# Optimization experiments

Hardware: AMD Instinct MI355X
Metric: run time of the kernel (lower is better)

Reference implementation:

```python
import jax, jax.numpy as jnp
import numpy as np

# config (stands in for global `args` in the original repo)
N = 8192            # args.tRNA + args.disease
NNZ = 262144        # number of edges in adj
N_SEEDS = 256
MASK_DEPTH = 2      # args.maskDepth
KEEP_RATE = 0.9     # args.keepRate


def setup_inputs() -> dict:
    rng = np.random.default_rng(0)
    # duplicate-free edge list (coalesced sparse tensor)
    h = rng.choice(N * N, size=NNZ, replace=False)
    adj_rows = jnp.asarray(h // N, dtype=jnp.int32)
    adj_cols = jnp.asarray(h % N, dtype=jnp.int32)
    key = jax.random.key(0)
    k1, k2, k3 = jax.random.split(key, 3)
    adj_values = jax.random.uniform(k1, (NNZ,), dtype=jnp.float32)
    seeds = jax.random.randint(k2, (N_SEEDS,), 0, N, dtype=jnp.int32)
    complemental = jax.random.uniform(k3, (N, N), dtype=jnp.float32)
    return {"adj_rows": adj_rows, "adj_cols": adj_cols, "adj_values": adj_values,
            "seeds": seeds, "complemental": complemental}


def _forward(adj_rows, adj_cols, adj_values, seeds, complemental):
    rows, cols = adj_rows, adj_cols
    # --- BFS edge masking (sequential per-seed removal == union removal) ---
    keep = jnp.ones((NNZ,), bool)
    seed_mask = jnp.zeros((N,), bool).at[seeds].set(True)
    mask_nodes = seed_mask
    for i in range(MASK_DEPTH):
        incident = keep & (seed_mask[rows] | seed_mask[cols])
        keep = keep & ~incident
        if i != MASK_DEPTH - 1:
            inc_i = incident.astype(jnp.int32)
            nxt = (jnp.zeros((N,), jnp.int32).at[rows].add(inc_i)
                   .at[cols].add(inc_i)) > 0
            seed_mask = nxt
            mask_nodes = mask_nodes | nxt
    # --- random node sampling augments the mask set ---
    key = jax.random.key(42)
    k1, k2, k3 = jax.random.split(key, 3)
    samp_num = int(N * KEEP_RATE)
    samped = jax.random.randint(k1, (samp_num,), 0, N)
    mask_nodes = mask_nodes.at[samped].set(True)
    # --- encoder adj: kept edges, values gathered from complemental, D^-1/2 A D^-1/2 ---
    keep_i = keep.astype(jnp.int32)
    enc_cov = (jnp.zeros((N, N), jnp.int32).at[rows, cols].add(keep_i)) > 0
    enc_dense = jnp.where(enc_cov, complemental, 0.0)
    deg = enc_dense.sum(axis=1)
    norm = (deg + 1e-12) ** -0.5
    enc = enc_dense * norm[:, None] * norm[None, :]
    # --- decoder adj: random mask-node pairs (symmetric) + self loops + kept edges ---
    mask_idx = jnp.nonzero(mask_nodes, size=N, fill_value=0)[0]
    tem_num = mask_nodes.sum()
    u1 = jax.random.uniform(k2, (NNZ,))
    u2 = jax.random.uniform(k3, (NNZ,))
    tem_rows = mask_idx[jnp.floor(u1 * tem_num).astype(jnp.int32)]
    tem_cols = mask_idx[jnp.floor(u2 * tem_num).astype(jnp.int32)]
    ar = jnp.arange(N, dtype=jnp.int32)
    new_rows = jnp.concatenate([tem_rows, tem_cols, ar, rows])
    new_cols = jnp.concatenate([tem_cols, tem_rows, ar, cols])
    valid = jnp.concatenate([jnp.ones((2 * NNZ + N,), jnp.int32), keep_i])
    # hash-dedup in the original == coverage set; values depend only on (r,c)
    dec_cov = (jnp.zeros((N, N), jnp.int32).at[new_rows, new_cols].add(valid)) > 0
    dec = jnp.where(dec_cov, complemental, 0.0)
    return enc, dec


def reference(adj_rows, adj_cols, adj_values, seeds, complemental):
    return _forward(adj_rows, adj_cols, adj_values, seeds, complemental)
```

## Files before the change

### kernel.cpp

```cpp
#include <hip/hip_runtime.h>
#include <stdint.h>
#include <math.h>

typedef float f4 __attribute__((ext_vector_type(4)));
typedef unsigned int u32;
typedef uint4 u32x4;

static __device__ __forceinline__ uint32_t rotl32(uint32_t x, int r) {
    return (x << r) | (x >> (32 - r));
}

static __device__ __forceinline__ void tf2x32(uint32_t k0, uint32_t k1,
                                              uint32_t& x0, uint32_t& x1) {
    uint32_t ks2 = k0 ^ k1 ^ 0x1BD11BDAu;
    x0 += k0; x1 += k1;
#define TFR(r) { x0 += x1; x1 = rotl32(x1, r); x1 ^= x0; }
    TFR(13) TFR(15) TFR(26) TFR(6)
    x0 += k1;  x1 += ks2 + 1u;
    TFR(17) TFR(29) TFR(16) TFR(24)
    x0 += ks2; x1 += k0 + 2u;
    TFR(13) TFR(15) TFR(26) TFR(6)
    x0 += k0;  x1 += k1 + 3u;
    TFR(17) TFR(29) TFR(16) TFR(24)
    x0 += k1;  x1 += ks2 + 4u;
    TFR(13) TFR(15) TFR(26) TFR(6)
    x0 += ks2; x1 += k0 + 5u;
#undef TFR
}

struct SubKeys { uint32_t k1a, k1b, k2a, k2b, k3a, k3b; };

static __device__ __forceinline__ SubKeys derive_keys() {
    uint32_t a0 = 0, b0 = 3; tf2x32(0u, 42u, a0, b0);
    uint32_t a1 = 1, b1 = 4; tf2x32(0u, 42u, a1, b1);
    uint32_t a2 = 2, b2 = 5; tf2x32(0u, 42u, a2, b2);
    SubKeys s; s.k1a = a0; s.k1b = a1; s.k2a = a2; s.k2b = b0; s.k3a = b1; s.k3b = b2;
    return s;
}

static __device__ __forceinline__ float bits_to_unit_float(uint32_t b) {
    return __uint_as_float((b >> 9) | 0x3f800000u) - 1.0f;
}

__global__ void k_seed(const int* __restrict__ seeds, int n_seeds,
                       unsigned char* __restrict__ seedm) {
    int i = blockIdx.x * blockDim.x + threadIdx.x;
    if (i < n_seeds) seedm[seeds[i]] = 1;
}

__global__ void k_edge1(const int* __restrict__ rows, const int* __restrict__ cols, int nnz,
                        const unsigned char* __restrict__ seedm,
                        unsigned char* __restrict__ keep, unsigned char* __restrict__ nxt) {
    int e = blockIdx.x * blockDim.x + threadIdx.x;
    if (e >= nnz) return;
    int r = rows[e], c = cols[e];
    bool inc = (seedm[r] | seedm[c]) != 0;
    keep[e] = inc ? 0 : 1;
    if (inc) { nxt[r] = 1; nxt[c] = 1; }
}

__global__ void k_edge2(const int* __restrict__ rows, const int* __restrict__ cols, int nnz,
                        const unsigned char* __restrict__ nxt,
                        unsigned char* __restrict__ keep) {
    int e = blockIdx.x * blockDim.x + threadIdx.x;
    if (e >= nnz) return;
    if (keep[e] && ((nxt[rows[e]] | nxt[cols[e]]) != 0)) keep[e] = 0;
}

__global__ void k_union(int n, const unsigned char* __restrict__ seedm,
                        const unsigned char* __restrict__ nxt,
                        unsigned char* __restrict__ mask) {
    int i = blockIdx.x * blockDim.x + threadIdx.x;
    if (i < n) mask[i] = (unsigned char)(seedm[i] | nxt[i]);
}

__global__ void k_samp(int half, int modmask, unsigned char* __restrict__ mask) {
    int t = blockIdx.x * blockDim.x + threadIdx.x;
    if (t >= half) return;
    SubKeys sk = derive_keys();
    uint32_t x0 = (uint32_t)t, x1 = (uint32_t)(t + half);
    tf2x32(sk.k1a, sk.k1b, x0, x1);
    mask[x0 & (uint32_t)modmask] = 1;
    mask[x1 & (uint32_t)modmask] = 1;
}

__global__ void __launch_bounds__(1024)
k_scan(int n, const unsigned char* __restrict__ mask,
       int* __restrict__ mask_idx, int* __restrict__ tem_num) {
    __shared__ int ssum[1024];
    int t = threadIdx.x;
    int per = n / 1024;
    int base = t * per;
    int loc[8];
    int s = 0;
    for (int j = 0; j < per; ++j) { loc[j] = mask[base + j]; s += loc[j]; }
    ssum[t] = s;
    __syncthreads();
    for (int off = 1; off < 1024; off <<= 1) {
        int v = (t >= off) ? ssum[t - off] : 0;
        __syncthreads();
        ssum[t] += v;
        __syncthreads();
    }
    int excl = ssum[t] - s;
    for (int j = 0; j < per; ++j)
        if (loc[j]) mask_idx[excl++] = base + j;
    if (t == 1023) *tem_num = ssum[1023];
}

__global__ void k_deg(const int* __restrict__ rows, const int* __restrict__ cols, int nnz,
                      const unsigned char* __restrict__ keep,
                      const float* __restrict__ comp, float* __restrict__ deg, int n) {
    int e = blockIdx.x * blockDim.x + threadIdx.x;
    if (e >= nnz) return;
    if (keep[e]) {
        int r = rows[e], c = cols[e];
        atomicAdd(&deg[r], comp[(size_t)r * n + c]);
    }
}

__global__ void k_norm(int n, const float* __restrict__ deg, float* __restrict__ nrm) {
    int i = blockIdx.x * blockDim.x + threadIdx.x;
    if (i < n) nrm[i] = 1.0f / sqrtf(deg[i] + 1e-12f);
}

#define WPR   256
#define WIN   262144
#define SLW   16384

__global__ void __launch_bounds__(256)
k_zslice(u32* __restrict__ decw) {
    u32x4* s4 = (u32x4*)(decw + (size_t)blockIdx.x * WIN);
    for (int i = threadIdx.x; i < SLW / 4; i += 256) {
        u32x4 z = {0u, 0u, 0u, 0u};
        s4[i] = z;
    }
}

__global__ void __launch_bounds__(256)
k_cov(const int* __restrict__ rows, const int* __restrict__ cols,
      int nnz, int n, int ehalf,
      const unsigned char* __restrict__ keep,
      const int* __restrict__ mask_idx, const int* __restrict__ tem_num,
      u32* __restrict__ decw) {
    int e = blockIdx.x * blockDim.x + threadIdx.x;
    if (e < nnz) {
        if (keep[e]) {
            int r = rows[e], c = cols[e];
            u32* base = decw + (size_t)(r >> 5) * WIN;
            int w = ((r & 31) << 8) + (c >> 5);
            u32 b = 1u << (c & 31);
            atomicOr(&base[w], b);
            atomicOr(&base[8192 + w], b);
        }
    } else if (e < nnz + n) {
        int i = e - nnz;
        atomicOr(&decw[(size_t)(i >> 5) * WIN + ((i & 31) << 8) + (i >> 5)],
                 1u << (i & 31));
    } else if (e < nnz + n + ehalf) {
        int q = e - nnz - n;
        SubKeys sk = derive_keys();
        float tf = (float)(*tem_num);
        uint32_t u1a = (uint32_t)q, u1b = (uint32_t)(q + ehalf);
        tf2x32(sk.k2a, sk.k2b, u1a, u1b);
        uint32_t u2a = (uint32_t)q, u2b = (uint32_t)(q + ehalf);
        tf2x32(sk.k3a, sk.k3b, u2a, u2b);
#pragma unroll
        for (int j = 0; j < 2; ++j) {
            uint32_t b1 = j ? u1b : u1a;
            uint32_t b2 = j ? u2b : u2a;
            int i1 = (int)(bits_to_unit_float(b1) * tf);
            int i2 = (int)(bits_to_unit_float(b2) * tf);
            int r = mask_idx[i1];
            int c = mask_idx[i2];
            atomicOr(&decw[(size_t)(r >> 5) * WIN + ((r & 31) << 8) + (c >> 5)],
                     1u << (c & 31));
            atomicOr(&decw[(size_t)(c >> 5) * WIN + ((c & 31) << 8) + (r >> 5)],
                     1u << (r & 31));
        }
    }
}

__global__ void __launch_bounds__(512)
k_dense2(int n, const float* __restrict__ comp, const float* __restrict__ nrm,
         float* __restrict__ enc, float* __restrict__ dec) {
    __shared__ u32 sdec[8192], senc[8192];
    const int t = threadIdx.x;
    const int b = blockIdx.x;
    {
        const u32x4* s4 = (const u32x4*)((const u32*)dec + (size_t)b * WIN);
        u32x4* ld = (u32x4*)sdec;
        u32x4* le = (u32x4*)senc;
        for (int i = t; i < SLW / 4; i += 512) {
            u32x4 v = s4[i];
            if (i < 2048) ld[i] = v; else le[i - 2048] = v;
        }
    }
    __syncthreads();
    const int base = b * 32;
    const f4* nrmv = (const f4*)nrm;
    for (int i = 0; i < 32; ++i) {
        int r = base + i;
        float nr = nrm[r];
        size_t rowo = (size_t)r * n;
        const f4* compv = (const f4*)(comp + rowo);
        f4* encv = (f4*)(enc + rowo);
        f4* decv = (f4*)(dec + rowo);
        int wrow = i << 8;
#pragma unroll
        for (int k = 0; k < 4; ++k) {
            int f = k * 512 + t;
            int sh = (f & 7) * 4;
            u32 ew = (senc[wrow + (f >> 3)] >> sh) & 0xFu;
            u32 dw = (sdec[wrow + (f >> 3)] >> sh) & 0xFu;
            f4 ev = {0.f, 0.f, 0.f, 0.f};
            f4 dv = {0.f, 0.f, 0.f, 0.f};
            if (ew | dw) {
                f4 cv = compv[f];
                if (dw & 1u) dv.x = cv.x;
                if (dw & 2u) dv.y = cv.y;
                if (dw & 4u) dv.z = cv.z;
                if (dw & 8u) dv.w = cv.w;
                if (ew) {
                    f4 nv = nrmv[f];
                    if (ew & 1u) ev.x = cv.x * nr * nv.x;
                    if (ew & 2u) ev.y = cv.y * nr * nv.y;
                    if (ew & 4u) ev.z = cv.z * nr * nv.z;
                    if (ew & 8u) ev.w = cv.w * nr * nv.w;
                }
            }
            __builtin_nontemporal_store(ev, &encv[f]);
            __builtin_nontemporal_store(dv, &decv[f]);
        }
    }
}

__global__ void k_enc(const int* __restrict__ rows, const int* __restrict__ cols, int nnz,
                      const unsigned char* __restrict__ keep,
                      const float* __restrict__ comp, const float* __restrict__ nrm,
                      float* __restrict__ enc, int n) {
    int e = blockIdx.x * blockDim.x + threadIdx.x;
    if (e >= nnz) return;
    if (keep[e]) {
        int r = rows[e], c = cols[e];
        size_t o = (size_t)r * n + c;
        enc[o] = comp[o] * nrm[r] * nrm[c];
    }
}

__global__ void k_dec_base(const int* __restrict__ rows, const int* __restrict__ cols,
                           int nnz, int n, const unsigned char* __restrict__ keep,
                           const float* __restrict__ comp, float* __restrict__ dec) {
    int e = blockIdx.x * blockDim.x + threadIdx.x;
    if (e < nnz) {
        if (keep[e]) {
            size_t o = (size_t)rows[e] * n + cols[e];
            dec[o] = comp[o];
        }
    } else if (e < nnz + n) {
        int i = e - nnz;
        size_t o = (size_t)i * n + i;
        dec[o] = comp[o];
    }
}

__global__ void k_dec_tem(int half, int n, const int* __restrict__ mask_idx,
                          const int* __restrict__ tem_num,
                          const float* __restrict__ comp, float* __restrict__ dec) {
    int e = blockIdx.x * blockDim.x + threadIdx.x;
    if (e >= half) return;
    SubKeys sk = derive_keys();
    float tf = (float)(*tem_num);
    uint32_t u1a = (uint32_t)e, u1b = (uint32_t)(e + half);
    tf2x32(sk.k2a, sk.k2b, u1a, u1b);
    uint32_t u2a = (uint32_t)e, u2b = (uint32_t)(e + half);
    tf2x32(sk.k3a, sk.k3b, u2a, u2b);
#pragma unroll
    for (int j = 0; j < 2; ++j) {
        uint32_t b1 = j ? u1b : u1a;
        uint32_t b2 = j ? u2b : u2a;
        int i1 = (int)(bits_to_unit_float(b1) * tf);
        int i2 = (int)(bits_to_unit_float(b2) * tf);
        int r = mask_idx[i1];
        int c = mask_idx[i2];
        size_t o1 = (size_t)r * n + c;
        size_t o2 = (size_t)c * n + r;
        dec[o1] = comp[o1];
        dec[o2] = comp[o2];
    }
}

extern "C" void kernel_launch(void* const* d_in, const int* in_sizes, int n_in,
                              void* d_out, int out_size, void* d_ws, size_t ws_size,
                              hipStream_t stream) {
    const int*   rows  = (const int*)d_in[0];
    const int*   cols  = (const int*)d_in[1];
    const int*   seeds = (const int*)d_in[3];
    const float* comp  = (const float*)d_in[4];

    const int nnz     = in_sizes[0];
    const int n_seeds = in_sizes[3];
    const int n       = (int)(sqrt((double)in_sizes[4]) + 0.5);

    float* enc = (float*)d_out;
    float* dec = enc + (size_t)n * n;

    char* ws = (char*)d_ws;
    float* deg            = (float*)(ws);
    float* nrm            = (float*)(ws + 4 * (size_t)n);
    int*   mask_idx       = (int*)  (ws + 8 * (size_t)n);
    int*   tem_num        = (int*)  (ws + 12 * (size_t)n);
    unsigned char* seedm  = (unsigned char*)(ws + 12 * (size_t)n + 256);
    unsigned char* nxt    = seedm + n;
    unsigned char* mask   = nxt + n;
    unsigned char* keep   = mask + n;

    const int B = 256;
    int samp_num = (int)((double)n * 0.9);
    int shalf = samp_num / 2;
    int ehalf = nnz / 2;

    size_t zbytes = 12 * (size_t)n + 256 + 3 * (size_t)n;
    hipMemsetAsync(d_ws, 0, zbytes, stream);

    k_seed <<<(n_seeds + B - 1) / B, B, 0, stream>>>(seeds, n_seeds, seedm);
    k_edge1<<<(nnz + B - 1) / B, B, 0, stream>>>(rows, cols, nnz, seedm, keep, nxt);
    k_edge2<<<(nnz + B - 1) / B, B, 0, stream>>>(rows, cols, nnz, nxt, keep);
    k_union<<<(n + B - 1) / B, B, 0, stream>>>(n, seedm, nxt, mask);
    k_samp <<<(shalf + B - 1) / B, B, 0, stream>>>(shalf, n - 1, mask);
    k_scan <<<1, 1024, 0, stream>>>(n, mask, mask_idx, tem_num);
    k_deg  <<<(nnz + B - 1) / B, B, 0, stream>>>(rows, cols, nnz, keep, comp, deg, n);
    k_norm <<<(n + B - 1) / B, B, 0, stream>>>(n, deg, nrm);

    if (n == 8192) {
        u32* decw = (u32*)dec;
        k_zslice<<<256, 256, 0, stream>>>(decw);
        int total = nnz + n + ehalf;
        k_cov   <<<(total + B - 1) / B, B, 0, stream>>>(rows, cols, nnz, n, ehalf,
                                                        keep, mask_idx, tem_num, decw);
        k_dense2<<<256, 512, 0, stream>>>(n, comp, nrm, enc, dec);
    } else {
        hipMemsetAsync(d_out, 0, 2 * (size_t)n * (size_t)n * sizeof(float), stream);
        k_enc  <<<(nnz + B - 1) / B, B, 0, stream>>>(rows, cols, nnz, keep, comp, nrm, enc, n);
        k_dec_base<<<(nnz + n + B - 1) / B, B, 0, stream>>>(rows, cols, nnz, n, keep, comp, dec);
        k_dec_tem<<<(ehalf + B - 1) / B, B, 0, stream>>>(ehalf, n, mask_idx, tem_num, comp, dec);
    }
}
```

Before: 751.6 us.

## Fuse edge masking with degree pass and shrink dense-pass tiles to 8 rows

Folds the second edge-mask pass and the degree accumulation into a single kernel, drops the union kernel by having the scan read the seed, next-frontier and a sampled bitmap directly, and writes sampled nodes as bits via atomicOr. The dense output kernel now handles 8 rows per block with 256 threads and 16KB of shared bitmap instead of 32 rows with 64KB, giving 1024 blocks rather than 256. This removes several launches and passes over the edge list, and is meant to improve occupancy and load balance of the dominant dense write kernel. The bitmap layout inside the decoder output is changed to match, at the cost of more blocks each loading a smaller slice.

```diff
diff --git a/kernel.cpp b/kernel.cpp
--- a/kernel.cpp
+++ b/kernel.cpp
@@ -59,33 +59,33 @@
     if (inc) { nxt[r] = 1; nxt[c] = 1; }
 }
 
-__global__ void k_edge2(const int* __restrict__ rows, const int* __restrict__ cols, int nnz,
-                        const unsigned char* __restrict__ nxt,
-                        unsigned char* __restrict__ keep) {
+__global__ void k_edge2deg(const int* __restrict__ rows, const int* __restrict__ cols,
+                           int nnz, int n,
+                           const unsigned char* __restrict__ nxt,
+                           unsigned char* __restrict__ keep,
+                           const float* __restrict__ comp, float* __restrict__ deg) {
     int e = blockIdx.x * blockDim.x + threadIdx.x;
     if (e >= nnz) return;
-    if (keep[e] && ((nxt[rows[e]] | nxt[cols[e]]) != 0)) keep[e] = 0;
-}
-
-__global__ void k_union(int n, const unsigned char* __restrict__ seedm,
-                        const unsigned char* __restrict__ nxt,
-                        unsigned char* __restrict__ mask) {
-    int i = blockIdx.x * blockDim.x + threadIdx.x;
-    if (i < n) mask[i] = (unsigned char)(seedm[i] | nxt[i]);
-}
-
-__global__ void k_samp(int half, int modmask, unsigned char* __restrict__ mask) {
+    int r = rows[e], c = cols[e];
+    bool kv = keep[e] && ((nxt[r] | nxt[c]) == 0);
+    keep[e] = kv ? 1 : 0;
+    if (kv) atomicAdd(&deg[r], comp[(size_t)r * n + c]);
+}
+
+__global__ void k_samp(int half, int modmask, u32* __restrict__ sampw) {
     int t = blockIdx.x * blockDim.x + threadIdx.x;
     if (t >= half) return;
     SubKeys sk = derive_keys();
     uint32_t x0 = (uint32_t)t, x1 = (uint32_t)(t + half);
     tf2x32(sk.k1a, sk.k1b, x0, x1);
-    mask[x0 & (uint32_t)modmask] = 1;
-    mask[x1 & (uint32_t)modmask] = 1;
+    x0 &= (uint32_t)modmask; x1 &= (uint32_t)modmask;
+    atomicOr(&sampw[x0 >> 5], 1u << (x0 & 31));
+    atomicOr(&sampw[x1 >> 5], 1u << (x1 & 31));
 }
 
 __global__ void __launch_bounds__(1024)
-k_scan(int n, const unsigned char* __restrict__ mask,
+k_scan(int n, const unsigned char* __restrict__ seedm,
+       const unsigned char* __restrict__ nxt, const u32* __restrict__ sampw,
        int* __restrict__ mask_idx, int* __restrict__ tem_num) {
     __shared__ int ssum[1024];
     int t = threadIdx.x;
@@ -93,7 +93,11 @@
     int base = t * per;
     int loc[8];
     int s = 0;
-    for (int j = 0; j < per; ++j) { loc[j] = mask[base + j]; s += loc[j]; }
+    for (int j = 0; j < per; ++j) {
+        int i = base + j;
+        int v = ((seedm[i] | nxt[i]) != 0) | ((sampw[i >> 5] >> (i & 31)) & 1u);
+        loc[j] = v; s += v;
+    }
     ssum[t] = s;
     __syncthreads();
     for (int off = 1; off < 1024; off <<= 1) {
@@ -108,33 +112,19 @@
     if (t == 1023) *tem_num = ssum[1023];
 }
 
-__global__ void k_deg(const int* __restrict__ rows, const int* __restrict__ cols, int nnz,
-                      const unsigned char* __restrict__ keep,
-                      const float* __restrict__ comp, float* __restrict__ deg, int n) {
-    int e = blockIdx.x * blockDim.x + threadIdx.x;
-    if (e >= nnz) return;
-    if (keep[e]) {
-        int r = rows[e], c = cols[e];
-        atomicAdd(&deg[r], comp[(size_t)r * n + c]);
-    }
-}
-
 __global__ void k_norm(int n, const float* __restrict__ deg, float* __restrict__ nrm) {
     int i = blockIdx.x * blockDim.x + threadIdx.x;
     if (i < n) nrm[i] = 1.0f / sqrtf(deg[i] + 1e-12f);
 }
 
-#define WPR   256
-#define WIN   262144
-#define SLW   16384
+#define WIN8  65536
+#define SLW8  4096
 
 __global__ void __launch_bounds__(256)
 k_zslice(u32* __restrict__ decw) {
-    u32x4* s4 = (u32x4*)(decw + (size_t)blockIdx.x * WIN);
-    for (int i = threadIdx.x; i < SLW / 4; i += 256) {
-        u32x4 z = {0u, 0u, 0u, 0u};
-        s4[i] = z;
-    }
+    u32x4* s4 = (u32x4*)(decw + (size_t)blockIdx.x * WIN8);
+    u32x4 z = {0u, 0u, 0u, 0u};
+    for (int i = threadIdx.x; i < SLW8 / 4; i += 256) s4[i] = z;
 }
 
 __global__ void __launch_bounds__(256)
@@ -147,15 +137,15 @@
     if (e < nnz) {
         if (keep[e]) {
             int r = rows[e], c = cols[e];
-            u32* base = decw + (size_t)(r >> 5) * WIN;
-            int w = ((r & 31) << 8) + (c >> 5);
+            u32* base = decw + (size_t)(r >> 3) * WIN8;
+            int w = ((r & 7) << 8) + (c >> 5);
             u32 b = 1u << (c & 31);
             atomicOr(&base[w], b);
-            atomicOr(&base[8192 + w], b);
+            atomicOr(&base[2048 + w], b);
         }
     } else if (e < nnz + n) {
         int i = e - nnz;
-        atomicOr(&decw[(size_t)(i >> 5) * WIN + ((i & 31) << 8) + (i >> 5)],
+        atomicOr(&decw[(size_t)(i >> 3) * WIN8 + ((i & 7) << 8) + (i >> 5)],
                  1u << (i & 31));
     } else if (e < nnz + n + ehalf) {
         int q = e - nnz - n;
@@ -173,33 +163,32 @@
             int i2 = (int)(bits_to_unit_float(b2) * tf);
             int r = mask_idx[i1];
             int c = mask_idx[i2];
-            atomicOr(&decw[(size_t)(r >> 5) * WIN + ((r & 31) << 8) + (c >> 5)],
+            atomicOr(&decw[(size_t)(r >> 3) * WIN8 + ((r & 7) << 8) + (c >> 5)],
                      1u << (c & 31));
-            atomicOr(&decw[(size_t)(c >> 5) * WIN + ((c & 31) << 8) + (r >> 5)],
+            atomicOr(&decw[(size_t)(c >> 3) * WIN8 + ((c & 7) << 8) + (r >> 5)],
                      1u << (r & 31));
         }
     }
 }
 
-__global__ void __launch_bounds__(512)
-k_dense2(int n, const float* __restrict__ comp, const float* __restrict__ nrm,
+__global__ void __launch_bounds__(256)
+k_dense3(int n, const float* __restrict__ comp, const float* __restrict__ nrm,
          float* __restrict__ enc, float* __restrict__ dec) {
-    __shared__ u32 sdec[8192], senc[8192];
+    __shared__ u32 sbm[SLW8];
     const int t = threadIdx.x;
     const int b = blockIdx.x;
     {
-        const u32x4* s4 = (const u32x4*)((const u32*)dec + (size_t)b * WIN);
-        u32x4* ld = (u32x4*)sdec;
-        u32x4* le = (u32x4*)senc;
-        for (int i = t; i < SLW / 4; i += 512) {
-            u32x4 v = s4[i];
-            if (i < 2048) ld[i] = v; else le[i - 2048] = v;
-        }
+        const u32x4* s4 = (const u32x4*)((const u32*)dec + (size_t)b * WIN8);
+        u32x4* l4 = (u32x4*)sbm;
+#pragma unroll
+        for (int i = 0; i < SLW8 / 4 / 256; ++i)
+            l4[i * 256 + t] = s4[i * 256 + t];
     }
     __syncthreads();
-    const int base = b * 32;
+    const int base = b * 8;
     const f4* nrmv = (const f4*)nrm;
-    for (int i = 0; i < 32; ++i) {
+#pragma unroll
+    for (int i = 0; i < 8; ++i) {
         int r = base + i;
         float nr = nrm[r];
         size_t rowo = (size_t)r * n;
@@ -208,11 +197,11 @@
         f4* decv = (f4*)(dec + rowo);
         int wrow = i << 8;
 #pragma unroll
-        for (int k = 0; k < 4; ++k) {
-            int f = k * 512 + t;
+        for (int k = 0; k < 8; ++k) {
+            int f = k * 256 + t;
             int sh = (f & 7) * 4;
-            u32 ew = (senc[wrow + (f >> 3)] >> sh) & 0xFu;
-            u32 dw = (sdec[wrow + (f >> 3)] >> sh) & 0xFu;
+            u32 dw = (sbm[wrow + (f >> 3)] >> sh) & 0xFu;
+            u32 ew = (sbm[2048 + wrow + (f >> 3)] >> sh) & 0xFu;
             f4 ev = {0.f, 0.f, 0.f, 0.f};
             f4 dv = {0.f, 0.f, 0.f, 0.f};
             if (ew | dw) {
@@ -310,35 +299,33 @@
     float* nrm            = (float*)(ws + 4 * (size_t)n);
     int*   mask_idx       = (int*)  (ws + 8 * (size_t)n);
     int*   tem_num        = (int*)  (ws + 12 * (size_t)n);
-    unsigned char* seedm  = (unsigned char*)(ws + 12 * (size_t)n + 256);
+    u32*   sampw          = (u32*)  (ws + 12 * (size_t)n + 256);
+    unsigned char* seedm  = (unsigned char*)(ws + 12 * (size_t)n + 256 + (size_t)n / 8);
     unsigned char* nxt    = seedm + n;
-    unsigned char* mask   = nxt + n;
-    unsigned char* keep   = mask + n;
+    unsigned char* keep   = nxt + n;
 
     const int B = 256;
     int samp_num = (int)((double)n * 0.9);
     int shalf = samp_num / 2;
     int ehalf = nnz / 2;
 
-    size_t zbytes = 12 * (size_t)n + 256 + 3 * (size_t)n;
+    size_t zbytes = 12 * (size_t)n + 256 + (size_t)n / 8 + 2 * (size_t)n;
     hipMemsetAsync(d_ws, 0, zbytes, stream);
 
-    k_seed <<<(n_seeds + B - 1) / B, B, 0, stream>>>(seeds, n_seeds, seedm);
-    k_edge1<<<(nnz + B - 1) / B, B, 0, stream>>>(rows, cols, nnz, seedm, keep, nxt);
-    k_edge2<<<(nnz + B - 1) / B, B, 0, stream>>>(rows, cols, nnz, nxt, keep);
-    k_union<<<(n + B - 1) / B, B, 0, stream>>>(n, seedm, nxt, mask);
-    k_samp <<<(shalf + B - 1) / B, B, 0, stream>>>(shalf, n - 1, mask);
-    k_scan <<<1, 1024, 0, stream>>>(n, mask, mask_idx, tem_num);
-    k_deg  <<<(nnz + B - 1) / B, B, 0, stream>>>(rows, cols, nnz, keep, comp, deg, n);
-    k_norm <<<(n + B - 1) / B, B, 0, stream>>>(n, deg, nrm);
+    k_seed    <<<(n_seeds + B - 1) / B, B, 0, stream>>>(seeds, n_seeds, seedm);
+    k_edge1   <<<(nnz + B - 1) / B, B, 0, stream>>>(rows, cols, nnz, seedm, keep, nxt);
+    k_samp    <<<(shalf + B - 1) / B, B, 0, stream>>>(shalf, n - 1, sampw);
+    k_edge2deg<<<(nnz + B - 1) / B, B, 0, stream>>>(rows, cols, nnz, n, nxt, keep, comp, deg);
+    k_scan    <<<1, 1024, 0, stream>>>(n, seedm, nxt, sampw, mask_idx, tem_num);
+    k_norm    <<<(n + B - 1) / B, B, 0, stream>>>(n, deg, nrm);
 
     if (n == 8192) {
         u32* decw = (u32*)dec;
-        k_zslice<<<256, 256, 0, stream>>>(decw);
+        k_zslice<<<n / 8, B, 0, stream>>>(decw);
         int total = nnz + n + ehalf;
         k_cov   <<<(total + B - 1) / B, B, 0, stream>>>(rows, cols, nnz, n, ehalf,
                                                         keep, mask_idx, tem_num, decw);
-        k_dense2<<<256, 512, 0, stream>>>(n, comp, nrm, enc, dec);
+        k_dense3<<<n / 8, B, 0, stream>>>(n, comp, nrm, enc, dec);
     } else {
         hipMemsetAsync(d_out, 0, 2 * (size_t)n * (size_t)n * sizeof(float), stream);
         k_enc  <<<(nnz + B - 1) / B, B, 0, stream>>>(rows, cols, nnz, keep, comp, nrm, enc, n);
```

New measurement: 735.8 us. -2.1%, faster.
